# Kernel tuning notes

Measured on AMD Instinct MI355X. Metric: run time of the kernel, lower is better.

Reference implementation:

```python
import jax, jax.numpy as jnp
import numpy as np

B, L, F, P = 128, 256, 4, 4   # dialogs, dialog length, future/past links
IN, H, C = 1024, 256, 7
N = B * L


def _build_edges():
    # same structure as build_intra_graph: self-loop + F future + P past per node
    i = np.arange(L)
    ss, tt = [], []
    for d in range(-P, F + 1):
        j = i + d
        m = (j >= 0) & (j < L)
        ss.append(i[m]); tt.append(j[m])
    s = np.concatenate(ss); t = np.concatenate(tt)
    offs = (np.arange(B) * L)[:, None]
    S = (s[None, :] + offs).ravel()
    T = (t[None, :] + offs).ravel()
    return np.stack([S, T]).astype(np.int32)


def setup_inputs() -> dict:
    key = jax.random.key(0)
    ks = jax.random.split(key, 16)
    ei = _build_edges()
    speakers = np.asarray(jax.random.randint(ks[0], (N,), 0, 2), dtype=np.int32)
    rel = (speakers[ei[0]] * speakers[ei[1]]).astype(np.int32)
    sd_in = 1.0 / np.sqrt(IN)
    sd_h = 1.0 / np.sqrt(H)
    return {
        "input": jax.random.normal(ks[1], (N, IN), jnp.float32),
        "dialog_lengths": jnp.full((B,), L, jnp.int32),
        "speakers": jnp.asarray(speakers),
        "labels": jax.random.randint(ks[2], (N,), 0, C, jnp.int32),
        "edge_index": jnp.asarray(ei),
        "rel_type": jnp.asarray(rel),
        # RGCNConv(IN, H, num_relations=2): per-relation weight, root weight, bias
        "W_rgcn": jax.random.normal(ks[3], (2, IN, H), jnp.float32) * sd_in,
        "W_root": jax.random.normal(ks[4], (IN, H), jnp.float32) * sd_in,
        "b_rgcn": jax.random.normal(ks[5], (H,), jnp.float32) * 0.01,
        # GraphConv(H, H): lin_rel (on aggregated neighbors, with bias), lin_root (no bias)
        "W_rel": jax.random.normal(ks[6], (H, H), jnp.float32) * sd_h,
        "b_rel": jax.random.normal(ks[7], (H,), jnp.float32) * 0.01,
        "W_grt": jax.random.normal(ks[8], (H, H), jnp.float32) * sd_h,
        # skip_con: Linear(IN, H)
        "W_skip": jax.random.normal(ks[9], (IN, H), jnp.float32) * sd_in,
        "b_skip": jax.random.normal(ks[10], (H,), jnp.float32) * 0.01,
        # classify: Linear(H, C)
        "W_cls": jax.random.normal(ks[11], (H, C), jnp.float32) * sd_h,
        "b_cls": jax.random.normal(ks[12], (C,), jnp.float32) * 0.01,
    }


def reference(input, dialog_lengths, speakers, labels, edge_index, rel_type,
              W_rgcn, W_root, b_rgcn, W_rel, b_rel, W_grt,
              W_skip, b_skip, W_cls, b_cls):
    n = input.shape[0]
    src, dst = edge_index[0], edge_index[1]
    seg = jax.ops.segment_sum

    # --- RGCNConv: out_i = x_i @ W_root + b + sum_r mean_{j in N_r(i)} x_j @ W_r
    t = jnp.einsum('ni,rio->rno', input, W_rgcn)      # [2, N, H]
    msg = t[rel_type, src]                            # [E, H] relation-specific messages
    h = input @ W_root + b_rgcn
    for r in range(2):
        m = (rel_type == r).astype(input.dtype)       # [E]
        s = seg(msg * m[:, None], dst, num_segments=n)
        cnt = seg(m, dst, num_segments=n)
        h = h + s / jnp.maximum(cnt, 1.0)[:, None]    # mean aggregation per relation

    # --- GraphConv (aggr='add'): out_i = W_rel @ sum_j h_j + b_rel + W_grt @ h_i
    neigh = seg(h[src], dst, num_segments=n)          # [N, H]
    h2 = neigh @ W_rel + b_rel + h @ W_grt

    # --- skip connection + classifier
    out = (h2 + input @ W_skip + b_skip) @ W_cls + b_cls  # [N, C]

    # --- cross entropy (mean)
    logp = jax.nn.log_softmax(out, axis=-1)
    loss = -jnp.mean(jnp.take_along_axis(logp, labels[:, None].astype(jnp.int32), axis=1))
    return out, loss
```

## Files before the change

### kernel.cpp

```cpp
#include <hip/hip_runtime.h>

#define NN 32768
#define INF 1024
#define HF 256

typedef __bf16 bf16x8 __attribute__((ext_vector_type(8)));
typedef float f32x4 __attribute__((ext_vector_type(4)));
typedef unsigned short u16x8 __attribute__((ext_vector_type(8)));

__device__ __forceinline__ float bf2f(unsigned short u) {
  union { unsigned int i; float f; } v; v.i = ((unsigned int)u) << 16; return v.f;
}
__device__ __forceinline__ unsigned short f2bf(float f) {
  union { float f; unsigned int i; } v; v.f = f;
  unsigned int x = v.i;
  return (unsigned short)((x + 0x7fffu + ((x >> 16) & 1u)) >> 16);
}

__device__ __forceinline__ void ld_lds16(const unsigned short* g, unsigned short* l) {
  __builtin_amdgcn_global_load_lds(
      (__attribute__((address_space(1))) const unsigned int*)g,
      (__attribute__((address_space(3))) unsigned int*)l, 16, 0, 0);
}

__global__ __launch_bounds__(256)
void diagcn_prep(const float* __restrict__ x, const float* __restrict__ Wrgcn,
                 const float* __restrict__ Wroot, const float* __restrict__ Wskip,
                 const float* __restrict__ Wgrt, const float* __restrict__ Wrel,
                 unsigned short* __restrict__ Xbf, unsigned short* __restrict__ WbigT,
                 unsigned short* __restrict__ WsmT, float* __restrict__ loss) {
  int bid = blockIdx.x;
  if (bid >= 288) {
    if (bid == 288 && threadIdx.x == 0) loss[0] = 0.f;
    int idx = (bid - 288) * 256 + threadIdx.x;
    const int stride = 2048 * 256;
#pragma unroll
    for (int it = 0; it < 16; ++it, idx += stride) {
      float4 v = ((const float4*)x)[idx];
      ushort4 u; u.x = f2bf(v.x); u.y = f2bf(v.y); u.z = f2bf(v.z); u.w = f2bf(v.w);
      ((ushort4*)Xbf)[idx] = u;
    }
    return;
  }
  __shared__ float tile[64 * 65];
  int tb = bid;
  const float* src;
  int k0, ncol0;
  unsigned short* dst;
  int ldd, nrow0;
  if (tb < 256) {
    int tn = tb >> 4, tk = tb & 15;
    int mat = tn >> 2;
    src = (mat == 0) ? Wrgcn : (mat == 1) ? (Wrgcn + 262144) : (mat == 2) ? Wroot : Wskip;
    k0 = tk * 64; ncol0 = (tn & 3) * 64;
    dst = WbigT; ldd = 1024; nrow0 = tn * 64;
  } else {
    int t2 = tb - 256;
    int tn = t2 >> 3, tk = t2 & 7;
    src = (tk < 4) ? Wgrt : Wrel;
    k0 = (tk & 3) * 64; ncol0 = tn * 64;
    dst = WsmT; ldd = 512; nrow0 = tn * 64;
  }
  int kdst0 = (tb < 256) ? k0 : (((tb - 256) & 7) * 64);
  int c = threadIdx.x & 63, rb = threadIdx.x >> 6;
#pragma unroll
  for (int it = 0; it < 16; ++it) {
    int r = rb + it * 4;
    tile[r * 65 + c] = src[(size_t)(k0 + r) * 256 + ncol0 + c];
  }
  __syncthreads();
  int kk = threadIdx.x & 63;
#pragma unroll
  for (int it = 0; it < 16; ++it) {
    int nn = rb + it * 4;
    dst[(size_t)(nrow0 + nn) * ldd + kdst0 + kk] = f2bf(tile[kk * 65 + nn]);
  }
}

__global__ __launch_bounds__(256)
void diagcn_gemm1(const unsigned short* __restrict__ A, const unsigned short* __restrict__ BT,
                  unsigned short* __restrict__ Y) {
  const int K = 1024;
  __shared__ unsigned short As[128 * 64];
  __shared__ unsigned short Bs[128 * 64];
  const int tid = threadIdx.x;
  const int w = tid >> 6, lane = tid & 63;
  const int wm = w >> 1, wn = w & 1;
  const int quad = lane >> 4, l15 = lane & 15;
  const int b = blockIdx.x;
  const int m0 = (((b & 7) << 5) + (b >> 6)) << 7;
  const int n0 = ((b >> 3) & 7) << 7;
  const int rowg = lane >> 3;
  const int kbsw = (lane & 7) ^ rowg;

  f32x4 acc[4][4] = {};
  const unsigned short* Abase = A + (size_t)m0 * K + kbsw * 8;
  const unsigned short* Bbase = BT + (size_t)n0 * K + kbsw * 8;

  for (int k0 = 0; k0 < K; k0 += 64) {
#pragma unroll
    for (int t = 0; t < 4; ++t) {
      int grp = w * 4 + t;
      int rl = grp * 8 + rowg;
      ld_lds16(Abase + (size_t)rl * K + k0, &As[grp * 512]);
      ld_lds16(Bbase + (size_t)rl * K + k0, &Bs[grp * 512]);
    }
    __syncthreads();
#pragma unroll
    for (int ks = 0; ks < 2; ++ks) {
      bf16x8 av[4], bv[4];
      int kb = ks * 4 + quad;
#pragma unroll
      for (int i = 0; i < 4; ++i) {
        int ra = wm * 64 + i * 16 + l15;
        int rb2 = wn * 64 + i * 16 + l15;
        av[i] = *(const bf16x8*)&As[ra * 64 + ((kb ^ (ra & 7)) << 3)];
        bv[i] = *(const bf16x8*)&Bs[rb2 * 64 + ((kb ^ (rb2 & 7)) << 3)];
      }
#pragma unroll
      for (int i = 0; i < 4; ++i)
#pragma unroll
        for (int j = 0; j < 4; ++j)
          acc[i][j] = __builtin_amdgcn_mfma_f32_16x16x32_bf16(av[i], bv[j], acc[i][j], 0, 0, 0);
    }
    __syncthreads();
  }
#pragma unroll
  for (int i = 0; i < 4; ++i)
#pragma unroll
    for (int j = 0; j < 4; ++j) {
      int row = m0 + wm * 64 + i * 16 + quad * 4;
      int col = n0 + wn * 64 + j * 16 + l15;
#pragma unroll
      for (int r = 0; r < 4; ++r)
        Y[(size_t)(row + r) * 1024 + col] = f2bf(acc[i][j][r]);
    }
}

__global__ __launch_bounds__(256)
void diagcn_hn(const unsigned short* __restrict__ Y, const int* __restrict__ spk,
               const float* __restrict__ brgcn, unsigned short* __restrict__ A2) {
  __shared__ unsigned short hl[24 * 256];
  const int b = blockIdx.x;
  const int nb = ((b & 7) << 12) + ((b >> 3) << 4);
  const int p0 = nb & 255, dbase = nb - p0;
  const int tid = threadIdx.x;
#pragma unroll
  for (int it = 0; it < 3; ++it) {
    int u = tid + it * 256;
    int r = u >> 5, cb = u & 31, c0 = cb << 3;
    int p = p0 - 4 + r;
    int pc = p < 0 ? 0 : (p > 255 ? 255 : p);
    int node = dbase + pc;
    int si = spk[node];
    float a0[8] = {}, a1[8] = {};
    float n0 = 0.f, n1 = 0.f;
#pragma unroll
    for (int d = -4; d <= 4; ++d) {
      int pj = p + d;
      float w = (pj >= 0 && pj < 256) ? 1.f : 0.f;
      int jc = pj < 0 ? 0 : (pj > 255 ? 255 : pj);
      int nj = dbase + jc;
      int rel = si & spk[nj];
      u16x8 v = *(const u16x8*)&Y[(size_t)nj * 1024 + (rel << 8) + c0];
      float w1 = rel ? w : 0.f, w0 = rel ? 0.f : w;
#pragma unroll
      for (int k = 0; k < 8; ++k) {
        float f = bf2f(v[k]);
        a0[k] += f * w0; a1[k] += f * w1;
      }
      n0 += w0; n1 += w1;
    }
    u16x8 vr = *(const u16x8*)&Y[(size_t)node * 1024 + 512 + c0];
    float i0 = 1.f / fmaxf(n0, 1.f), i1 = 1.f / fmaxf(n1, 1.f);
    u16x8 uo;
#pragma unroll
    for (int k = 0; k < 8; ++k)
      uo[k] = f2bf(bf2f(vr[k]) + brgcn[c0 + k] + a0[k] * i0 + a1[k] * i1);
    *(u16x8*)&hl[r * 256 + c0] = uo;
    if (r >= 4 && r < 20)
      *(u16x8*)&A2[(size_t)(dbase + p) * 512 + c0] = uo;
  }
  __syncthreads();
#pragma unroll
  for (int it = 0; it < 2; ++it) {
    int u = tid + it * 256;
    int r = u >> 5, cb = u & 31, c0 = cb << 3;
    int p = p0 + r;
    float s[8] = {};
#pragma unroll
    for (int d = -4; d <= 4; ++d) {
      int pj = p + d;
      float w = (pj >= 0 && pj < 256) ? 1.f : 0.f;
      u16x8 v = *(const u16x8*)&hl[(r + 4 + d) * 256 + c0];
#pragma unroll
      for (int k = 0; k < 8; ++k) s[k] += bf2f(v[k]) * w;
    }
    u16x8 uo;
#pragma unroll
    for (int k = 0; k < 8; ++k) uo[k] = f2bf(s[k]);
    *(u16x8*)&A2[(size_t)(nb + r) * 512 + 256 + c0] = uo;
  }
}

__global__ __launch_bounds__(256)
void diagcn_gemm2(const unsigned short* __restrict__ A, const unsigned short* __restrict__ BT,
                  const unsigned short* __restrict__ Y, const float* __restrict__ Wcls,
                  const float* __restrict__ bcls, const float* __restrict__ brel,
                  const float* __restrict__ bskip, const int* __restrict__ labels,
                  float* __restrict__ out, float* __restrict__ loss) {
  const int K = 512;
  __shared__ unsigned short As[64 * 64];
  __shared__ unsigned short Bs[256 * 64];
  __shared__ float Wc[2312];
  for (int i = threadIdx.x; i < 2312; i += 256) {
    float v;
    if (i < 1792) v = Wcls[i];
    else if (i < 1799) v = bcls[i - 1792];
    else if (i < 1800) v = 0.f;
    else if (i < 2056) v = brel[i - 1800];
    else v = bskip[i - 2056];
    Wc[i] = v;
  }
  const int tid = threadIdx.x;
  const int w = tid >> 6, lane = tid & 63;
  const int quad = lane >> 4, l15 = lane & 15;
  const int b = blockIdx.x;
  const int m0 = (((b & 7) << 6) + (b >> 3)) << 6;
  const int rowg = lane >> 3;
  const int kbsw = (lane & 7) ^ rowg;

  f32x4 acc[16] = {};
  const unsigned short* Abase = A + (size_t)m0 * K + kbsw * 8;
  const unsigned short* Bbase = BT + kbsw * 8;

  for (int k0 = 0; k0 < K; k0 += 64) {
#pragma unroll
    for (int t = 0; t < 2; ++t) {
      int grp = w * 2 + t;
      ld_lds16(Abase + (size_t)(grp * 8 + rowg) * K + k0, &As[grp * 512]);
    }
#pragma unroll
    for (int t = 0; t < 8; ++t) {
      int grp = w * 8 + t;
      ld_lds16(Bbase + (size_t)(grp * 8 + rowg) * K + k0, &Bs[grp * 512]);
    }
    __syncthreads();
#pragma unroll
    for (int ks = 0; ks < 2; ++ks) {
      int kb = ks * 4 + quad;
      int ra = w * 16 + l15;
      bf16x8 av = *(const bf16x8*)&As[ra * 64 + ((kb ^ (ra & 7)) << 3)];
#pragma unroll
      for (int j = 0; j < 16; ++j) {
        int rb2 = j * 16 + l15;
        bf16x8 bv = *(const bf16x8*)&Bs[rb2 * 64 + ((kb ^ (rb2 & 7)) << 3)];
        acc[j] = __builtin_amdgcn_mfma_f32_16x16x32_bf16(av, bv, acc[j], 0, 0, 0);
      }
    }
    __syncthreads();
  }

  unsigned short* Ysk = Bs;
  {
    int row2 = w * 2 + (lane >> 5);
    const unsigned short* ysrc = Y + (size_t)(m0 + row2) * 1024 + 768 + (lane & 31) * 8;
#pragma unroll
    for (int pS = 0; pS < 8; ++pS)
      ld_lds16(ysrc + (size_t)pS * 8 * 1024, &Ysk[(pS * 8 + w * 2) * 256]);
  }
  __syncthreads();

  float wsum[4][7] = {};
#pragma unroll
  for (int j = 0; j < 16; ++j) {
    int col = j * 16 + l15;
    float bb = Wc[1800 + col] + Wc[2056 + col];
#pragma unroll
    for (int r = 0; r < 4; ++r) {
      int lrow = w * 16 + quad * 4 + r;
      float z = acc[j][r] + bb + bf2f(Ysk[lrow * 256 + col]);
#pragma unroll
      for (int c = 0; c < 7; ++c) wsum[r][c] += z * Wc[col * 7 + c];
    }
  }
#pragma unroll
  for (int o = 1; o < 16; o <<= 1)
#pragma unroll
    for (int r = 0; r < 4; ++r)
#pragma unroll
      for (int c = 0; c < 7; ++c) wsum[r][c] += __shfl_xor(wsum[r][c], o, 64);

  float lsum = 0.f;
#pragma unroll
  for (int r = 0; r < 4; ++r) {
    int row = m0 + w * 16 + quad * 4 + r;
    float o7[7], mx = -1e30f;
#pragma unroll
    for (int c = 0; c < 7; ++c) {
      o7[c] = wsum[r][c] + Wc[1792 + c];
      mx = fmaxf(mx, o7[c]);
    }
    if (l15 < 7) out[(size_t)row * 7 + l15] = o7[l15];
    float s = 0.f;
#pragma unroll
    for (int c = 0; c < 7; ++c) s += expf(o7[c] - mx);
    int lab = labels[row];
    lsum += mx + logf(s) - o7[lab];
  }
  lsum += __shfl_xor(lsum, 16, 64);
  lsum += __shfl_xor(lsum, 32, 64);
  if (lane == 0) atomicAdd(loss, lsum * (1.0f / (float)NN));
}

extern "C" void kernel_launch(void* const* d_in, const int* in_sizes, int n_in,
                              void* d_out, int out_size, void* d_ws, size_t ws_size,
                              hipStream_t stream) {
  const float* x      = (const float*)d_in[0];
  const int* speakers = (const int*)d_in[2];
  const int* labels   = (const int*)d_in[3];
  const float* Wrgcn  = (const float*)d_in[6];
  const float* Wroot  = (const float*)d_in[7];
  const float* brgcn  = (const float*)d_in[8];
  const float* Wrel   = (const float*)d_in[9];
  const float* brel   = (const float*)d_in[10];
  const float* Wgrt   = (const float*)d_in[11];
  const float* Wskip  = (const float*)d_in[12];
  const float* bskip  = (const float*)d_in[13];
  const float* Wcls   = (const float*)d_in[14];
  const float* bcls   = (const float*)d_in[15];
  float* out = (float*)d_out;
  float* loss = out + (size_t)NN * 7;

  const size_t OFF_XBF  = 0;
  const size_t OFF_WBIG = 67108864;
  const size_t OFF_WSM  = 69206016;
  const size_t OFF_Y    = 69468160;
  const size_t OFF_A2   = 136577024;
  const size_t NEED     = 170131456;
  if (ws_size < NEED) return;

  char* ws = (char*)d_ws;
  unsigned short* Xbf   = (unsigned short*)(ws + OFF_XBF);
  unsigned short* WbigT = (unsigned short*)(ws + OFF_WBIG);
  unsigned short* WsmT  = (unsigned short*)(ws + OFF_WSM);
  unsigned short* Y     = (unsigned short*)(ws + OFF_Y);
  unsigned short* A2    = (unsigned short*)(ws + OFF_A2);

  diagcn_prep<<<dim3(2336), dim3(256), 0, stream>>>(x, Wrgcn, Wroot, Wskip, Wgrt, Wrel,
                                                    Xbf, WbigT, WsmT, loss);
  diagcn_gemm1<<<dim3(2048), dim3(256), 0, stream>>>(Xbf, WbigT, Y);
  diagcn_hn<<<dim3(2048), dim3(256), 0, stream>>>(Y, speakers, brgcn, A2);
  diagcn_gemm2<<<dim3(512), dim3(256), 0, stream>>>(A2, WsmT, Y, Wcls, bcls, brel, bskip,
                                                    labels, out, loss);
}
```

Baseline: 394.2 us.

## Fuse fp32-to-bf16 input conversion into GEMM1 A-tile loading

Removes the separate pass that converted the fp32 input to a bf16 workspace copy. GEMM1 now reads fp32 rows directly, converts them in registers and writes swizzled bf16 into LDS, replacing the async global-to-LDS loads for A. This saves writing and re-reading a 64MB intermediate. In exchange, each of the 8 column blocks rereads the fp32 input (twice the bytes of bf16), and the A loads become synchronous register loads, so they no longer overlap as well with MFMA work.

```diff
diff --git a/kernel.cpp b/kernel.cpp
--- a/kernel.cpp
+++ b/kernel.cpp
@@ -24,26 +24,14 @@
 }
 
 __global__ __launch_bounds__(256)
-void diagcn_prep(const float* __restrict__ x, const float* __restrict__ Wrgcn,
-                 const float* __restrict__ Wroot, const float* __restrict__ Wskip,
-                 const float* __restrict__ Wgrt, const float* __restrict__ Wrel,
-                 unsigned short* __restrict__ Xbf, unsigned short* __restrict__ WbigT,
-                 unsigned short* __restrict__ WsmT, float* __restrict__ loss) {
-  int bid = blockIdx.x;
-  if (bid >= 288) {
-    if (bid == 288 && threadIdx.x == 0) loss[0] = 0.f;
-    int idx = (bid - 288) * 256 + threadIdx.x;
-    const int stride = 2048 * 256;
-#pragma unroll
-    for (int it = 0; it < 16; ++it, idx += stride) {
-      float4 v = ((const float4*)x)[idx];
-      ushort4 u; u.x = f2bf(v.x); u.y = f2bf(v.y); u.z = f2bf(v.z); u.w = f2bf(v.w);
-      ((ushort4*)Xbf)[idx] = u;
-    }
-    return;
-  }
+void diagcn_prep(const float* __restrict__ Wrgcn, const float* __restrict__ Wroot,
+                 const float* __restrict__ Wskip, const float* __restrict__ Wgrt,
+                 const float* __restrict__ Wrel,
+                 unsigned short* __restrict__ WbigT, unsigned short* __restrict__ WsmT,
+                 float* __restrict__ loss) {
+  int tb = blockIdx.x;
+  if (tb == 0 && threadIdx.x == 0) loss[0] = 0.f;
   __shared__ float tile[64 * 65];
-  int tb = bid;
   const float* src;
   int k0, ncol0;
   unsigned short* dst;
@@ -78,7 +66,7 @@
 }
 
 __global__ __launch_bounds__(256)
-void diagcn_gemm1(const unsigned short* __restrict__ A, const unsigned short* __restrict__ BT,
+void diagcn_gemm1(const float* __restrict__ X, const unsigned short* __restrict__ BT,
                   unsigned short* __restrict__ Y) {
   const int K = 1024;
   __shared__ unsigned short As[128 * 64];
@@ -93,8 +81,12 @@
   const int rowg = lane >> 3;
   const int kbsw = (lane & 7) ^ rowg;
 
+  const int ar = tid >> 1;
+  const int ah = tid & 1;
+  const float4* Xrow = (const float4*)(X + (size_t)(m0 + ar) * 1024) + ah * 8;
+  unsigned short* Asw = &As[ar * 64];
+
   f32x4 acc[4][4] = {};
-  const unsigned short* Abase = A + (size_t)m0 * K + kbsw * 8;
   const unsigned short* Bbase = BT + (size_t)n0 * K + kbsw * 8;
 
   for (int k0 = 0; k0 < K; k0 += 64) {
@@ -102,8 +94,21 @@
     for (int t = 0; t < 4; ++t) {
       int grp = w * 4 + t;
       int rl = grp * 8 + rowg;
-      ld_lds16(Abase + (size_t)rl * K + k0, &As[grp * 512]);
       ld_lds16(Bbase + (size_t)rl * K + k0, &Bs[grp * 512]);
+    }
+    {
+      float4 f[8];
+#pragma unroll
+      for (int c = 0; c < 8; ++c) f[c] = Xrow[(k0 >> 2) + c];
+#pragma unroll
+      for (int c = 0; c < 4; ++c) {
+        int kb = ah * 4 + c;
+        float4 lo = f[c * 2], hi = f[c * 2 + 1];
+        bf16x8 v;
+        v[0] = (__bf16)lo.x; v[1] = (__bf16)lo.y; v[2] = (__bf16)lo.z; v[3] = (__bf16)lo.w;
+        v[4] = (__bf16)hi.x; v[5] = (__bf16)hi.y; v[6] = (__bf16)hi.z; v[7] = (__bf16)hi.w;
+        *(bf16x8*)&Asw[(kb ^ (ar & 7)) << 3] = v;
+      }
     }
     __syncthreads();
 #pragma unroll
@@ -332,24 +337,22 @@
   float* out = (float*)d_out;
   float* loss = out + (size_t)NN * 7;
 
-  const size_t OFF_XBF  = 0;
-  const size_t OFF_WBIG = 67108864;
-  const size_t OFF_WSM  = 69206016;
-  const size_t OFF_Y    = 69468160;
-  const size_t OFF_A2   = 136577024;
-  const size_t NEED     = 170131456;
+  const size_t OFF_WBIG = 0;
+  const size_t OFF_WSM  = 2097152;
+  const size_t OFF_Y    = 2359296;
+  const size_t OFF_A2   = 69468160;
+  const size_t NEED     = 103022592;
   if (ws_size < NEED) return;
 
   char* ws = (char*)d_ws;
-  unsigned short* Xbf   = (unsigned short*)(ws + OFF_XBF);
   unsigned short* WbigT = (unsigned short*)(ws + OFF_WBIG);
   unsigned short* WsmT  = (unsigned short*)(ws + OFF_WSM);
   unsigned short* Y     = (unsigned short*)(ws + OFF_Y);
   unsigned short* A2    = (unsigned short*)(ws + OFF_A2);
 
-  diagcn_prep<<<dim3(2336), dim3(256), 0, stream>>>(x, Wrgcn, Wroot, Wskip, Wgrt, Wrel,
-                                                    Xbf, WbigT, WsmT, loss);
-  diagcn_gemm1<<<dim3(2048), dim3(256), 0, stream>>>(Xbf, WbigT, Y);
+  diagcn_prep<<<dim3(288), dim3(256), 0, stream>>>(Wrgcn, Wroot, Wskip, Wgrt, Wrel,
+                                                   WbigT, WsmT, loss);
+  diagcn_gemm1<<<dim3(2048), dim3(256), 0, stream>>>(x, WbigT, Y);
   diagcn_hn<<<dim3(2048), dim3(256), 0, stream>>>(Y, speakers, brgcn, A2);
   diagcn_gemm2<<<dim3(512), dim3(256), 0, stream>>>(A2, WsmT, Y, Wcls, bcls, brel, bskip,
                                                     labels, out, loss);
```

Measured after the change: 453.7 us. +15.1%, slower.
